# Kernel tuning notes

Hardware: AMD Instinct MI355X
Metric: run time of the kernel (lower is better)

The kernel has to match this reference:

```python
import jax, jax.numpy as jnp
import numpy as np

B, N, E, H = 2, 2048, 2048, 16
D = E // H  # head_dim = 128


def setup_inputs() -> dict:
    key = jax.random.key(0)
    k1, k2, k3, k4 = jax.random.split(key, 4)
    x = jax.random.normal(k1, (B, N, E), dtype=jnp.float32)
    Wq = jax.random.normal(k2, (E, E), dtype=jnp.float32) * 0.02
    Wkv = jax.random.normal(k3, (2 * E, E), dtype=jnp.float32) * 0.02
    Wout = jax.random.normal(k4, (E, E), dtype=jnp.float32) * 0.02
    return {"x": x, "Wq": Wq, "Wkv": Wkv, "Wout": Wout}


def reference(x, Wq, Wkv, Wout):
    # projections (torch Linear: y = x @ W.T)
    q = x @ Wq.T                      # [b, n, e]
    kv = x @ Wkv.T                    # [b, n, 2e]
    k, v = jnp.split(kv, 2, axis=-1)  # each [b, n, e]

    def split_heads(t):
        return t.reshape(B, N, H, D).transpose(0, 2, 1, 3)  # [b, h, n, d]

    q, k, v = split_heads(q), split_heads(k), split_heads(v)

    scale = D ** -0.5
    sim = jnp.einsum('bhid,bhjd->bhij', q * scale, k)  # [b, h, n, n]

    # causal mask: triu(j - i + 1) masks strictly-future positions
    mask_value = -jnp.finfo(sim.dtype).max
    causal_mask = jnp.triu(jnp.ones((N, N), dtype=bool), k=1)
    sim = jnp.where(causal_mask, mask_value, sim)

    attn = jax.nn.softmax(sim, axis=-1)
    out = jnp.einsum('bhij,bhjd->bhid', attn, v)  # [b, h, n, d]
    out = out.transpose(0, 2, 1, 3).reshape(B, N, E)
    return out @ Wout.T
```

## Files before the change

### kernel.cpp

```cpp
#include <hip/hip_runtime.h>


typedef __bf16 bf16;
typedef bf16 bf16x2 __attribute__((ext_vector_type(2)));
typedef bf16 bf16x4 __attribute__((ext_vector_type(4)));
typedef bf16 bf16x8 __attribute__((ext_vector_type(8)));
typedef float f32x4 __attribute__((ext_vector_type(4)));
typedef float f32x16 __attribute__((ext_vector_type(16)));

typedef const __attribute__((address_space(1))) void cg_void;
typedef __attribute__((address_space(3))) void lds_void;

#define MFMA16(a, b, c) __builtin_amdgcn_mfma_f32_16x16x32_bf16((a), (b), (c), 0, 0, 0)
#define MFMA32(a, b, c) __builtin_amdgcn_mfma_f32_32x32x16_bf16((a), (b), (c), 0, 0, 0)

__device__ __forceinline__ void async_load16(const bf16* g, bf16* l) {
  __builtin_amdgcn_global_load_lds((cg_void*)g, (lds_void*)l, 16, 0, 0);
}

__global__ __launch_bounds__(256) void cast_all_kernel(
    const float* __restrict__ x, const float* __restrict__ wq,
    const float* __restrict__ wkv, const float* __restrict__ wout,
    bf16* __restrict__ xb, bf16* __restrict__ wqkvb, bf16* __restrict__ woutb) {
  long i = (long)blockIdx.x * 256 + threadIdx.x;
  const float* src; bf16* dst; long off;
  if (i < 1048576)      { src = x;    dst = xb;            off = i; }
  else if (i < 2621440) { src = wq;   dst = wqkvb;         off = i - 1048576;
                          if (off >= 524288) { src = wkv; dst = wqkvb + 4194304; off -= 524288; } }
  else                  { src = wout; dst = woutb;         off = i - 2621440; }
  float4 f0 = ((const float4*)src)[2 * off];
  float4 f1 = ((const float4*)src)[2 * off + 1];
  bf16x8 o;
  o[0] = (bf16)f0.x; o[1] = (bf16)f0.y; o[2] = (bf16)f0.z; o[3] = (bf16)f0.w;
  o[4] = (bf16)f1.x; o[5] = (bf16)f1.y; o[6] = (bf16)f1.z; o[7] = (bf16)f1.w;
  ((bf16x8*)dst)[off] = o;
}

template <typename OutT, bool SPLITV>
__global__ __launch_bounds__(256, 4)
void gemm_bt_kernel(const bf16* __restrict__ A, const bf16* __restrict__ B,
                    OutT* __restrict__ C, int K, int NN, bf16* __restrict__ vt) {
  __shared__ __attribute__((aligned(16))) bf16 smem[8192];
  bf16* As = smem;
  bf16* Bs = smem + 4096;
  const int tid = threadIdx.x;
  const int wave = tid >> 6, lane = tid & 63;
  const int quad = lane >> 4, l15 = lane & 15;
  const int m0 = blockIdx.y * 128, n0 = blockIdx.x * 128;
  const int wm = (wave >> 1) * 64, wn = (wave & 1) * 64;

  f32x4 acc[4][4];
#pragma unroll
  for (int i = 0; i < 4; ++i)
#pragma unroll
    for (int j = 0; j < 4; ++j) acc[i][j] = {0.f, 0.f, 0.f, 0.f};

  const int srow = tid >> 2;
  const int scol = (tid & 3) * 8;
  const bf16* aG = A + (size_t)(m0 + srow) * K + scol;
  const bf16* bG = B + (size_t)(n0 + srow) * K + scol;
  bf16* aL = As + srow * 32 + scol;
  bf16* bL = Bs + srow * 32 + scol;
  const size_t gstep = (size_t)64 * K;

  for (int kt = 0; kt < K; kt += 32) {
    __syncthreads();
    async_load16(aG, aL);
    async_load16(aG + gstep, aL + 64 * 32);
    async_load16(bG, bL);
    async_load16(bG + gstep, bL + 64 * 32);
    aG += 32; bG += 32;
    __syncthreads();

    bf16x8 af[4], bfr[4];
#pragma unroll
    for (int i = 0; i < 4; ++i)
      af[i] = *(const bf16x8*)(As + (wm + i * 16 + l15) * 32 + quad * 8);
#pragma unroll
    for (int j = 0; j < 4; ++j)
      bfr[j] = *(const bf16x8*)(Bs + (wn + j * 16 + l15) * 32 + quad * 8);
#pragma unroll
    for (int i = 0; i < 4; ++i)
#pragma unroll
      for (int j = 0; j < 4; ++j) acc[i][j] = MFMA16(af[i], bfr[j], acc[i][j]);
  }

  if (SPLITV && n0 >= 4096) {
    const int f0 = n0 - 4096;
    const int b = m0 >> 11;
    const int nbase = m0 & 2047;
#pragma unroll
    for (int p = 0; p < 2; ++p) {
      __syncthreads();
      if ((wave >> 1) == p) {
#pragma unroll
        for (int i = 0; i < 4; ++i)
#pragma unroll
          for (int r = 0; r < 4; ++r) {
            int nl = i * 16 + quad * 4 + r;
#pragma unroll
            for (int j = 0; j < 4; ++j) {
              int f = wn + j * 16 + l15;
              smem[nl * 128 + ((((f >> 3) + nl) & 15) * 8) + (f & 7)] = (bf16)acc[i][j][r];
            }
          }
      }
      __syncthreads();
#pragma unroll
      for (int c = 0; c < 4; ++c) {
        int idx = c * 256 + tid;
        int f = idx >> 3, n8 = idx & 7;
        bf16x8 o;
#pragma unroll
        for (int k = 0; k < 8; ++k) {
          int nl = n8 * 8 + k;
          o[k] = smem[nl * 128 + ((((f >> 3) + nl) & 15) * 8) + (f & 7)];
        }
        *(bf16x8*)(vt + ((size_t)(b * 2048 + f0 + f)) * 2048 + nbase + p * 64 + n8 * 8) = o;
      }
    }
    return;
  }

#pragma unroll
  for (int i = 0; i < 4; ++i) {
#pragma unroll
    for (int r = 0; r < 4; ++r) {
      int row = m0 + wm + i * 16 + quad * 4 + r;
      size_t base = (size_t)row * NN + n0 + wn + l15;
#pragma unroll
      for (int j = 0; j < 4; ++j) C[base + j * 16] = (OutT)acc[i][j][r];
    }
  }
}

__global__ __launch_bounds__(256, 2)
void attn_kernel(const bf16* __restrict__ qk, const bf16* __restrict__ vt,
                 bf16* __restrict__ yb) {
  constexpr int NSEQ = 2048, E = 2048, QKS = 4096;
  __shared__ __attribute__((aligned(16))) bf16 Ks[2][64 * 128];
  __shared__ __attribute__((aligned(16))) bf16 Vs[2][128 * 64];
  const int tid = threadIdx.x;
  const int wave = tid >> 6, lane = tid & 63;
  const int l31 = lane & 31, half = lane >> 5;
  const int id = blockIdx.x;
  const int slot = (id >> 5) & 15;
  const int bh = (id & 7) | (((id >> 3) & 3) << 3);
  const int b = bh >> 4, h = bh & 15;
  const int qt = (slot < 8) ? slot : 23 - slot;
  const float c1 = 0.08838834764831845f * 1.44269504088896f;

  const int krow_s = tid >> 4, kch_s = tid & 15;
  const int vrow_s = tid >> 3, vch_s = tid & 7;
  const bf16* kg = qk + (size_t)(b * NSEQ) * QKS + 2048 + h * 128;
  const bf16* vg = vt + (size_t)b * E * NSEQ + (size_t)(h * 128) * NSEQ;

  const int diag = 2 * qt + (wave >> 1);
  const int ktmax = 2 * qt + 1;

  {
    bf16* kdst = Ks[0] + tid * 8;
    bf16* vdst = Vs[0] + tid * 8;
#pragma unroll
    for (int p = 0; p < 4; ++p) {
      int r = p * 16 + krow_s;
      async_load16(kg + (size_t)r * QKS + (kch_s ^ (r & 7)) * 8, kdst + p * 2048);
    }
#pragma unroll
    for (int p = 0; p < 4; ++p) {
      int r = p * 32 + vrow_s;
      async_load16(vg + (size_t)r * NSEQ + (vch_s ^ (r & 7)) * 8, vdst + p * 2048);
    }
  }

  const int qrow = qt * 128 + wave * 32 + l31;
  bf16x8 qf[8];
  {
    const bf16* qp = qk + (size_t)(b * NSEQ + qrow) * QKS + h * 128 + half * 8;
#pragma unroll
    for (int k8 = 0; k8 < 8; ++k8) qf[k8] = *(const bf16x8*)(qp + k8 * 16);
  }

  float m = -3.0e38f, l = 0.f;
  f32x16 accO[4];
#pragma unroll
  for (int md = 0; md < 4; ++md)
#pragma unroll
    for (int r = 0; r < 16; ++r) accO[md][r] = 0.f;

  union PU { unsigned u; bf16x2 h; };
  union FU { bf16x8 v; unsigned u[4]; };

  for (int kt = 0; kt <= ktmax; ++kt) {
    const int cur = kt & 1;
    __syncthreads();

    if (kt < ktmax) {
      const int nxt = kt + 1;
      bf16* kdst = Ks[1 - cur] + tid * 8;
      bf16* vdst = Vs[1 - cur] + tid * 8;
#pragma unroll
      for (int p = 0; p < 4; ++p) {
        int r = p * 16 + krow_s;
        async_load16(kg + (size_t)(nxt * 64 + r) * QKS + (kch_s ^ (r & 7)) * 8, kdst + p * 2048);
      }
#pragma unroll
      for (int p = 0; p < 4; ++p) {
        int r = p * 32 + vrow_s;
        async_load16(vg + (size_t)r * NSEQ + nxt * 64 + (vch_s ^ (r & 7)) * 8, vdst + p * 2048);
      }
    }

    if (kt > diag) continue;

    const bf16* ks = Ks[cur];
    const bf16* vs = Vs[cur];

    f32x16 st[2];
#pragma unroll
    for (int mt = 0; mt < 2; ++mt)
#pragma unroll
      for (int r = 0; r < 16; ++r) st[mt][r] = 0.f;
#pragma unroll
    for (int k8 = 0; k8 < 8; ++k8) {
#pragma unroll
      for (int mt = 0; mt < 2; ++mt) {
        int row = mt * 32 + l31;
        int sl = (k8 * 2 + half) ^ (row & 7);
        bf16x8 kf = *(const bf16x8*)(ks + row * 128 + sl * 8);
        st[mt] = MFMA32(kf, qf[k8], st[mt]);
      }
    }

    if (kt == diag) {
#pragma unroll
      for (int mt = 0; mt < 2; ++mt)
#pragma unroll
        for (int r = 0; r < 16; ++r) {
          int t = kt * 64 + mt * 32 + (r & 3) + 8 * (r >> 2) + 4 * half;
          if (t > qrow) st[mt][r] = -3.0e38f;
        }
    }

    float mx = -3.0e38f;
#pragma unroll
    for (int mt = 0; mt < 2; ++mt)
#pragma unroll
      for (int r = 0; r < 16; ++r) mx = fmaxf(mx, st[mt][r]);
    mx = fmaxf(mx, __shfl_xor(mx, 32));
    float mnew = fmaxf(m, mx);
    float alpha = exp2f((m - mnew) * c1);
    float mc = mnew * c1;
    m = mnew;

    float psum = 0.f;
    unsigned pown[2][4][2];
#pragma unroll
    for (int mt = 0; mt < 2; ++mt)
#pragma unroll
      for (int qd = 0; qd < 4; ++qd)
#pragma unroll
        for (int pr = 0; pr < 2; ++pr) {
          float p0 = exp2f(st[mt][qd * 4 + pr * 2] * c1 - mc);
          float p1 = exp2f(st[mt][qd * 4 + pr * 2 + 1] * c1 - mc);
          psum += p0 + p1;
          PU a; a.h[0] = (bf16)p0; a.h[1] = (bf16)p1;
          pown[mt][qd][pr] = a.u;
        }
    psum += __shfl_xor(psum, 32);
    l = l * alpha + psum;

#pragma unroll
    for (int md = 0; md < 4; ++md)
#pragma unroll
      for (int r = 0; r < 16; ++r) accO[md][r] *= alpha;

#pragma unroll
    for (int mt = 0; mt < 2; ++mt)
#pragma unroll
      for (int c = 0; c < 2; ++c) {
        const int qa = 2 * c, qb = 2 * c + 1;
        unsigned ra0 = __shfl_xor(pown[mt][qa][0], 32);
        unsigned ra1 = __shfl_xor(pown[mt][qa][1], 32);
        unsigned rb0 = __shfl_xor(pown[mt][qb][0], 32);
        unsigned rb1 = __shfl_xor(pown[mt][qb][1], 32);
        FU f;
        f.u[0] = half ? rb0 : pown[mt][qa][0];
        f.u[1] = half ? rb1 : pown[mt][qa][1];
        f.u[2] = half ? pown[mt][qb][0] : ra0;
        f.u[3] = half ? pown[mt][qb][1] : ra1;
        const int kk = mt * 2 + c;
#pragma unroll
        for (int md = 0; md < 4; ++md) {
          int row = md * 32 + l31;
          bf16x8 vf = *(const bf16x8*)(vs + row * 64 + (((kk * 2 + half) ^ (row & 7)) * 8));
          accO[md] = MFMA32(vf, f.v, accO[md]);
        }
      }
  }

  float invl = 1.0f / l;
  bf16* yp = yb + (size_t)(b * NSEQ + qrow) * E + h * 128;
#pragma unroll
  for (int md = 0; md < 4; ++md)
#pragma unroll
    for (int rq = 0; rq < 4; ++rq) {
      bf16x4 o;
#pragma unroll
      for (int i = 0; i < 4; ++i) o[i] = (bf16)(accO[md][rq * 4 + i] * invl);
      *(bf16x4*)(yp + md * 32 + rq * 8 + half * 4) = o;
    }
}

extern "C" void kernel_launch(void* const* d_in, const int* in_sizes, int n_in,
                              void* d_out, int out_size, void* d_ws, size_t ws_size,
                              hipStream_t stream) {
  const float* x    = (const float*)d_in[0];
  const float* Wq   = (const float*)d_in[1];
  const float* Wkv  = (const float*)d_in[2];
  const float* Wout = (const float*)d_in[3];
  float* out = (float*)d_out;

  constexpr size_t NX = (size_t)2 * 2048 * 2048;
  constexpr size_t NW = (size_t)2048 * 2048;

  bf16* xb     = (bf16*)d_ws;
  bf16* wqkvb  = xb + NX;
  bf16* woutb  = wqkvb + 3 * NW;
  bf16* qk_b   = woutb + NW;
  bf16* y_b    = qk_b + 2 * NX;
  bf16* vt_b   = y_b + NX;

  cast_all_kernel<<<12288, 256, 0, stream>>>(x, Wq, Wkv, Wout, xb, wqkvb, woutb);

  gemm_bt_kernel<bf16, true><<<dim3(48, 32), 256, 0, stream>>>(
      xb, wqkvb, qk_b, 2048, 4096, vt_b);
  attn_kernel<<<512, 256, 0, stream>>>(qk_b, vt_b, y_b);
  gemm_bt_kernel<float, false><<<dim3(16, 32), 256, 0, stream>>>(
      y_b, woutb, out, 2048, 2048, nullptr);
}
```

Baseline: 384.2 us.

## Replace QKV projection GEMM with 256x256-tile, 8-wave pipelined kernel

Adds a dedicated QKV projection kernel that uses 256x256 output tiles, 512 threads, and a 64-wide K step. It double-buffers LDS with XOR-swizzled async global-to-LDS loads, staged across four MFMA sub-phases, and uses setprio around the MFMA bursts. The V-transpose epilogue is rewritten to use a swizzled LDS tile with vector reads, and blocks are remapped for L2 locality. This aims to raise arithmetic intensity and overlap loads with compute compared with the 128x128 tile GEMM. The trade-off is heavier register and LDS use, which may limit occupancy.

```diff
diff --git a/kernel.cpp b/kernel.cpp
--- a/kernel.cpp
+++ b/kernel.cpp
@@ -36,10 +36,143 @@
   ((bf16x8*)dst)[off] = o;
 }
 
-template <typename OutT, bool SPLITV>
+#define STAGE_A(bufi, h, tt) do {                              \
+    const bf16* g_ = Ag + (h) * 262144 + (tt) * 64;            \
+    bf16* d_ = ldsA + (bufi) * 16384 + (h) * 8192;             \
+    async_load16(g_, d_);                                      \
+    async_load16(g_ + 131072, d_ + 4096);                      \
+  } while (0)
+#define STAGE_B(bufi, h, tt) do {                              \
+    const bf16* g_ = Bg + (h) * 262144 + (tt) * 64;            \
+    bf16* d_ = ldsB + (bufi) * 16384 + (h) * 8192;             \
+    async_load16(g_, d_);                                      \
+    async_load16(g_ + 131072, d_ + 4096);                      \
+  } while (0)
+
+__global__ __launch_bounds__(512, 2)
+void gemm_qkv_8phase(const bf16* __restrict__ A, const bf16* __restrict__ B,
+                     bf16* __restrict__ qk, bf16* __restrict__ vt) {
+  __shared__ __attribute__((aligned(16))) bf16 sm[2][2][256][64];
+  const int tid = threadIdx.x;
+  const int lane = tid & 63;
+  const int wid = tid >> 6;
+  const int quad = lane >> 4, l15 = lane & 15;
+  const int wr = wid >> 2, wc = wid & 3;
+
+  const int lb = (blockIdx.x & 7) * 48 + (blockIdx.x >> 3);
+  const int bn = lb % 24, bm = lb / 24;
+  const int m0 = bm * 256, n0 = bn * 256;
+
+  const int srow = tid >> 3;
+  const int kswz8 = ((tid & 7) ^ (srow & 7)) * 8;
+  const bf16* Ag = A + (size_t)(m0 + srow) * 2048 + kswz8;
+  const bf16* Bg = B + (size_t)(n0 + srow) * 2048 + kswz8;
+  bf16* ldsA = &sm[0][0][0][0] + tid * 8;
+  bf16* ldsB = &sm[1][0][0][0] + tid * 8;
+
+  f32x4 acc[8][4];
+#pragma unroll
+  for (int i = 0; i < 8; ++i)
+#pragma unroll
+    for (int j = 0; j < 4; ++j) acc[i][j] = {0.f, 0.f, 0.f, 0.f};
+
+  const int r7 = l15 & 7;
+  const int c0 = (quad ^ r7) * 8;
+  const int c1 = ((4 + quad) ^ r7) * 8;
+  const int arow = (wr * 128 + l15) * 64;
+  const int brow = (wc * 64 + l15) * 64;
+
+  STAGE_A(0, 0, 0); STAGE_A(0, 1, 0); STAGE_B(0, 0, 0); STAGE_B(0, 1, 0);
+  STAGE_A(1, 0, 1);
+  asm volatile("s_waitcnt vmcnt(2)" ::: "memory");
+  __builtin_amdgcn_s_barrier();
+
+  for (int t = 0; t < 32; ++t) {
+    const int cur = t & 1;
+    const bf16* as = &sm[0][0][0][0] + cur * 16384;
+    const bf16* bs = &sm[1][0][0][0] + cur * 16384;
+#pragma unroll
+    for (int q = 0; q < 4; ++q) {
+      const int fi = (q >> 1) * 4, fj = (q & 1) * 2;
+      bf16x8 af[4][2], bfr[2][2];
+#pragma unroll
+      for (int i = 0; i < 4; ++i) {
+        af[i][0] = *(const bf16x8*)(as + arow + (fi + i) * 1024 + c0);
+        af[i][1] = *(const bf16x8*)(as + arow + (fi + i) * 1024 + c1);
+      }
+#pragma unroll
+      for (int j = 0; j < 2; ++j) {
+        bfr[j][0] = *(const bf16x8*)(bs + brow + (fj + j) * 1024 + c0);
+        bfr[j][1] = *(const bf16x8*)(bs + brow + (fj + j) * 1024 + c1);
+      }
+      if (t < 31) {
+        const int nb = 1 - cur;
+        if (q == 0) STAGE_A(nb, 1, t + 1);
+        if (q == 1) STAGE_B(nb, 0, t + 1);
+        if (q == 2) STAGE_B(nb, 1, t + 1);
+      }
+      __builtin_amdgcn_s_barrier();
+      asm volatile("s_waitcnt lgkmcnt(0)" ::: "memory");
+      __builtin_amdgcn_s_setprio(1);
+#pragma unroll
+      for (int ks = 0; ks < 2; ++ks)
+#pragma unroll
+        for (int i = 0; i < 4; ++i)
+#pragma unroll
+          for (int j = 0; j < 2; ++j)
+            acc[fi + i][fj + j] = MFMA16(af[i][ks], bfr[j][ks], acc[fi + i][fj + j]);
+      __builtin_amdgcn_s_setprio(0);
+      __builtin_amdgcn_s_barrier();
+    }
+    if (t < 30) {
+      STAGE_A(cur, 0, t + 2);
+      asm volatile("s_waitcnt vmcnt(2)" ::: "memory");
+      __builtin_amdgcn_s_barrier();
+    } else if (t == 30) {
+      asm volatile("s_waitcnt vmcnt(0)" ::: "memory");
+      __builtin_amdgcn_s_barrier();
+    }
+  }
+
+  if (n0 < 4096) {
+#pragma unroll
+    for (int i = 0; i < 8; ++i)
+#pragma unroll
+      for (int r = 0; r < 4; ++r) {
+        const size_t base = (size_t)(m0 + wr * 128 + i * 16 + quad * 4 + r) * 4096
+                          + n0 + wc * 64 + l15;
+#pragma unroll
+        for (int j = 0; j < 4; ++j) qk[base + j * 16] = (bf16)acc[i][j][r];
+      }
+  } else {
+    __syncthreads();
+    bf16* T = &sm[0][0][0][0];
+#pragma unroll
+    for (int i = 0; i < 8; ++i)
+#pragma unroll
+      for (int r = 0; r < 4; ++r) {
+        const int nl = wr * 128 + i * 16 + quad * 4 + r;
+#pragma unroll
+        for (int j = 0; j < 4; ++j) {
+          const int fl = wc * 64 + j * 16 + l15;
+          T[fl * 256 + ((((nl >> 3) ^ (fl & 31)) << 3) | (nl & 7))] = (bf16)acc[i][j][r];
+        }
+      }
+    __syncthreads();
+    const int f0g = n0 - 4096, nb0 = m0 & 2047, b = m0 >> 11;
+#pragma unroll
+    for (int c = 0; c < 16; ++c) {
+      const int idx = c * 512 + tid;
+      const int fl = idx >> 5, nb = idx & 31;
+      bf16x8 o = *(const bf16x8*)(T + fl * 256 + ((nb ^ (fl & 31)) << 3));
+      *(bf16x8*)(vt + (size_t)(b * 2048 + f0g + fl) * 2048 + nb0 + nb * 8) = o;
+    }
+  }
+}
+
 __global__ __launch_bounds__(256, 4)
-void gemm_bt_kernel(const bf16* __restrict__ A, const bf16* __restrict__ B,
-                    OutT* __restrict__ C, int K, int NN, bf16* __restrict__ vt) {
+void gemm_out_kernel(const bf16* __restrict__ A, const bf16* __restrict__ B,
+                     float* __restrict__ C, int K, int NN) {
   __shared__ __attribute__((aligned(16))) bf16 smem[8192];
   bf16* As = smem;
   bf16* Bs = smem + 4096;
@@ -85,43 +218,6 @@
       for (int j = 0; j < 4; ++j) acc[i][j] = MFMA16(af[i], bfr[j], acc[i][j]);
   }
 
-  if (SPLITV && n0 >= 4096) {
-    const int f0 = n0 - 4096;
-    const int b = m0 >> 11;
-    const int nbase = m0 & 2047;
-#pragma unroll
-    for (int p = 0; p < 2; ++p) {
-      __syncthreads();
-      if ((wave >> 1) == p) {
-#pragma unroll
-        for (int i = 0; i < 4; ++i)
-#pragma unroll
-          for (int r = 0; r < 4; ++r) {
-            int nl = i * 16 + quad * 4 + r;
-#pragma unroll
-            for (int j = 0; j < 4; ++j) {
-              int f = wn + j * 16 + l15;
-              smem[nl * 128 + ((((f >> 3) + nl) & 15) * 8) + (f & 7)] = (bf16)acc[i][j][r];
-            }
-          }
-      }
-      __syncthreads();
-#pragma unroll
-      for (int c = 0; c < 4; ++c) {
-        int idx = c * 256 + tid;
-        int f = idx >> 3, n8 = idx & 7;
-        bf16x8 o;
-#pragma unroll
-        for (int k = 0; k < 8; ++k) {
-          int nl = n8 * 8 + k;
-          o[k] = smem[nl * 128 + ((((f >> 3) + nl) & 15) * 8) + (f & 7)];
-        }
-        *(bf16x8*)(vt + ((size_t)(b * 2048 + f0 + f)) * 2048 + nbase + p * 64 + n8 * 8) = o;
-      }
-    }
-    return;
-  }
-
 #pragma unroll
   for (int i = 0; i < 4; ++i) {
 #pragma unroll
@@ -129,7 +225,7 @@
       int row = m0 + wm + i * 16 + quad * 4 + r;
       size_t base = (size_t)row * NN + n0 + wn + l15;
 #pragma unroll
-      for (int j = 0; j < 4; ++j) C[base + j * 16] = (OutT)acc[i][j][r];
+      for (int j = 0; j < 4; ++j) C[base + j * 16] = (float)acc[i][j][r];
     }
   }
 }
@@ -333,9 +429,7 @@
 
   cast_all_kernel<<<12288, 256, 0, stream>>>(x, Wq, Wkv, Wout, xb, wqkvb, woutb);
 
-  gemm_bt_kernel<bf16, true><<<dim3(48, 32), 256, 0, stream>>>(
-      xb, wqkvb, qk_b, 2048, 4096, vt_b);
+  gemm_qkv_8phase<<<384, 512, 0, stream>>>(xb, wqkvb, qk_b, vt_b);
   attn_kernel<<<512, 256, 0, stream>>>(qk_b, vt_b, y_b);
-  gemm_bt_kernel<float, false><<<dim3(16, 32), 256, 0, stream>>>(
-      y_b, woutb, out, 2048, 2048, nullptr);
-}
+  gemm_out_kernel<<<dim3(16, 32), 256, 0, stream>>>(y_b, woutb, out, 2048, 2048);
+}
```

Result: no change. 388.2 us (+1.0%).
